# Kernel optimization log

Hardware: AMD Instinct MI355X
Metric: run time of the kernel (lower is better)

## Reference

```python
import jax, jax.numpy as jnp
import numpy as np

L, B, E = 512, 4, 256
SCALE = 0.05  # keep sigmoid in a non-saturated range


def setup_inputs() -> dict:
    key = jax.random.key(0)
    ks = jax.random.split(key, 6)
    return {
        "emb": jax.random.normal(ks[0], (L, B, E), dtype=jnp.float32),
        "w1": jax.random.normal(ks[1], (E, E), dtype=jnp.float32) * SCALE,
        "w2": jax.random.normal(ks[2], (E, E), dtype=jnp.float32) * SCALE,
        "w3": jax.random.normal(ks[3], (E, E), dtype=jnp.float32) * SCALE,
        "b3": jax.random.normal(ks[4], (E,), dtype=jnp.float32) * SCALE,
        "w0": jax.random.normal(ks[5], (E,), dtype=jnp.float32) * SCALE,
    }


def reference(emb, w1, w2, w3, b3, w0):
    # emb: (L, B, E). torch Linear computes x @ W.T (+ b).
    Lq = emb.shape[0]
    u = jnp.einsum('lbe,fe->lbf', emb, w1)                      # w1(x_i), per key i
    q = jnp.einsum('lbe,fe->lbf', emb, w2)                      # w2(x_t), per query t
    c = jnp.einsum('lbe,fe->lbf', jnp.cumsum(emb, axis=0), w3) + b3  # w3(cumsum up to t)
    # gate[t, i, b, e] = sigmoid(u[i] + q[t] + c[t]); additive score via w0
    gate = jax.nn.sigmoid(u[None, :, :, :] + (q + c)[:, None, :, :])  # (L, L, B, E)
    scores = jnp.einsum('tibe,e->tib', gate, w0)                # (L, L, B)
    causal = jnp.tril(jnp.ones((Lq, Lq), dtype=emb.dtype))      # i <= t
    scores = scores * causal[:, :, None]
    # m_a[t] = sum_{i<=t} a_i * x_i
    return jnp.einsum('tib,ibe->tbe', scores, emb)              # (L, B, E)
```

## Files before the change

### kernel.cpp

```cpp
#include <hip/hip_runtime.h>
#include <hip/hip_bf16.h>

#define L_  512
#define B_  4
#define E_  256
#define TT  8
#define TI  64
#define CH  16
#define ROWS_PER_CH (L_ / CH)

typedef unsigned short u16;

#define NLOG2E (-1.44269504f)

__device__ __forceinline__ float bflo(unsigned u) { return __uint_as_float(u << 16); }
__device__ __forceinline__ float bfhi(unsigned u) { return __uint_as_float(u & 0xffff0000u); }

__device__ __forceinline__ unsigned pack_bf2(float x, float y) {
  __hip_bfloat162 h = __float22bfloat162_rn(make_float2(x, y));
  return *reinterpret_cast<unsigned*>(&h);
}

__device__ __forceinline__ float sigs(float xs) {
  float e = __builtin_amdgcn_exp2f(xs);
  return __builtin_amdgcn_rcpf(1.0f + e);
}

__global__ __launch_bounds__(256) void gemm3_k(
    const float* __restrict__ A,
    const float* __restrict__ w1, const float* __restrict__ w2, const float* __restrict__ w3,
    float* __restrict__ o1, float* __restrict__ o2, float* __restrict__ o3) {
  __shared__ float As[64 * 32], Ws[64 * 32];
  const int tid = threadIdx.x, tx = tid & 15, ty = tid >> 4;
  const int r0 = blockIdx.x * 64, f0 = blockIdx.y * 64, z = blockIdx.z;
  const float* W = (z == 0) ? w1 : (z == 1) ? w2 : w3;
  float* O = (z == 0) ? o1 : (z == 1) ? o2 : o3;
  float acc[4][4] = {};
  for (int kb = 0; kb < 256; kb += 32) {
    for (int j = 0; j < 2; ++j) {
      int idx = j * 256 + tid;
      int r = idx >> 3, g = idx & 7;
      float4 av = *(const float4*)(A + (size_t)(r0 + r) * E_ + kb + g * 4);
      float4 wv = *(const float4*)(W + (size_t)(f0 + r) * E_ + kb + g * 4);
      int gs = g ^ ((r >> 2) & 7);
      *(float4*)(As + r * 32 + gs * 4) = av;
      *(float4*)(Ws + r * 32 + gs * 4) = wv;
    }
    __syncthreads();
#pragma unroll
    for (int g = 0; g < 8; ++g) {
      float4 a[4], w[4];
#pragma unroll
      for (int i = 0; i < 4; ++i) {
        int r = ty * 4 + i;
        a[i] = *(const float4*)(As + r * 32 + (g ^ ((r >> 2) & 7)) * 4);
        int f = tx * 4 + i;
        w[i] = *(const float4*)(Ws + f * 32 + (g ^ ((f >> 2) & 7)) * 4);
      }
#pragma unroll
      for (int i = 0; i < 4; ++i)
#pragma unroll
        for (int j = 0; j < 4; ++j)
          acc[i][j] += a[i].x * w[j].x + a[i].y * w[j].y + a[i].z * w[j].z + a[i].w * w[j].w;
    }
    __syncthreads();
  }
  const float scl = (z == 0) ? NLOG2E : 1.0f;
#pragma unroll
  for (int i = 0; i < 4; ++i) {
    float4 v = make_float4(acc[i][0] * scl, acc[i][1] * scl, acc[i][2] * scl, acc[i][3] * scl);
    *(float4*)(O + (size_t)(r0 + ty * 4 + i) * E_ + f0 + tx * 4) = v;
  }
}

__global__ __launch_bounds__(256) void scanA_k(
    const float* __restrict__ v3, float* __restrict__ tot) {
  const int e = threadIdx.x, c = blockIdx.x, b = blockIdx.y;
  float s = 0.f;
  for (int l = c * ROWS_PER_CH; l < (c + 1) * ROWS_PER_CH; ++l)
    s += v3[((size_t)l * B_ + b) * E_ + e];
  tot[((size_t)c * B_ + b) * E_ + e] = s;
}

__global__ __launch_bounds__(256) void scanB_k(
    const float* __restrict__ v3, float* __restrict__ q2qc,
    const float* __restrict__ b3, const float* __restrict__ tot) {
  const int e = threadIdx.x, c = blockIdx.x, b = blockIdx.y;
  float run = 0.f;
  for (int cc = 0; cc < c; ++cc)
    run += tot[((size_t)cc * B_ + b) * E_ + e];
  const float bb = b3[e];
  for (int l = c * ROWS_PER_CH; l < (c + 1) * ROWS_PER_CH; ++l) {
    size_t o = ((size_t)l * B_ + b) * E_ + e;
    run += v3[o];
    q2qc[o] = NLOG2E * (q2qc[o] + bb + run);
  }
}

__device__ __forceinline__ void stage_tile_bf16(const float* __restrict__ src_base,
                                                u16* tile, int tid) {
#pragma unroll
  for (int c = 0; c < 16; ++c) {
    int idx = c * 256 + tid;
    int r = idx >> 6, col4 = idx & 63;
    float4 v = *(const float4*)(src_base + (size_t)r * (B_ * E_) + col4 * 4);
    unsigned p0 = pack_bf2(v.x, v.y);
    unsigned p1 = pack_bf2(v.z, v.w);
    *(uint2*)(tile + r * 264 + col4 * 4) = make_uint2(p0, p1);
  }
}

__global__ __launch_bounds__(256) void attn_main_k(
    const float* __restrict__ emb, const float* __restrict__ U,
    const float* __restrict__ QC, const float* __restrict__ w0g,
    float* __restrict__ out) {
  const int tt = blockIdx.x, ic = blockIdx.y, b = blockIdx.z;
  const int t0 = tt * TT, i0 = ic * TI;
  if (i0 > t0 + TT - 1) return;

  __shared__ u16 tile[TI * 264];
  __shared__ float s_s[TT][TI];
  const int tid = threadIdx.x;
  const int wave = tid >> 6, lane = tid & 63;

  stage_tile_bf16(U + ((size_t)i0 * B_ + b) * E_, tile, tid);
  __syncthreads();

#pragma unroll
  for (int tl = 0; tl < 2; ++tl) {
    int t = t0 + wave * 2 + tl;
    float acc0 = 0.f, acc1 = 0.f, acc2 = 0.f, acc3 = 0.f;
    if (t >= i0) {
      int row = __builtin_amdgcn_readfirstlane(t * B_ + b);
      const float* qcrow = QC + (size_t)row * E_;
      const u16* urow = tile + lane * 264;
#pragma unroll 4
      for (int g = 0; g < 32; ++g) {
        uint4 raw = *(const uint4*)(urow + g * 8);
        float4 q0 = *(const float4*)(qcrow + g * 8);
        float4 q1 = *(const float4*)(qcrow + g * 8 + 4);
        float4 z0 = *(const float4*)(w0g + g * 8);
        float4 z1 = *(const float4*)(w0g + g * 8 + 4);
        acc0 += z0.x * sigs(bflo(raw.x) + q0.x);
        acc1 += z0.y * sigs(bfhi(raw.x) + q0.y);
        acc2 += z0.z * sigs(bflo(raw.y) + q0.z);
        acc3 += z0.w * sigs(bfhi(raw.y) + q0.w);
        acc0 += z1.x * sigs(bflo(raw.z) + q1.x);
        acc1 += z1.y * sigs(bfhi(raw.z) + q1.y);
        acc2 += z1.z * sigs(bflo(raw.w) + q1.z);
        acc3 += z1.w * sigs(bfhi(raw.w) + q1.w);
      }
    }
    float s = (acc0 + acc1) + (acc2 + acc3);
    if (i0 + lane > t) s = 0.f;
    s_s[wave * 2 + tl][lane] = s;
  }
  __syncthreads();

  stage_tile_bf16(emb + ((size_t)i0 * B_ + b) * E_, tile, tid);
  __syncthreads();

#pragma unroll
  for (int tl = 0; tl < 2; ++tl) {
    int t = t0 + wave * 2 + tl;
    if (t < i0) continue;
    float4 o = make_float4(0.f, 0.f, 0.f, 0.f);
    const int nI = min(TI, t - i0 + 1);
    const float* srow = &s_s[wave * 2 + tl][0];
    for (int i = 0; i < nI; ++i) {
      float s = srow[i];
      uint2 raw = *(const uint2*)(tile + i * 264 + lane * 4);
      o.x += s * bflo(raw.x);
      o.y += s * bfhi(raw.x);
      o.z += s * bflo(raw.y);
      o.w += s * bfhi(raw.y);
    }
    float* op = out + ((size_t)t * B_ + b) * E_ + lane * 4;
    atomicAdd(op + 0, o.x);
    atomicAdd(op + 1, o.y);
    atomicAdd(op + 2, o.z);
    atomicAdd(op + 3, o.w);
  }
}

extern "C" void kernel_launch(void* const* d_in, const int* in_sizes, int n_in,
                              void* d_out, int out_size, void* d_ws, size_t ws_size,
                              hipStream_t stream) {
  const float* emb = (const float*)d_in[0];
  const float* w1  = (const float*)d_in[1];
  const float* w2  = (const float*)d_in[2];
  const float* w3  = (const float*)d_in[3];
  const float* b3  = (const float*)d_in[4];
  const float* w0  = (const float*)d_in[5];
  float* out = (float*)d_out;

  float* U   = (float*)d_ws;
  float* Q2  = U + 524288;
  float* V3  = Q2 + 524288;
  float* TOT = V3 + 524288;

  hipMemsetAsync(out, 0, (size_t)524288 * sizeof(float), stream);
  gemm3_k<<<dim3(32, 4, 3), 256, 0, stream>>>(emb, w1, w2, w3, U, Q2, V3);
  scanA_k<<<dim3(CH, B_), 256, 0, stream>>>(V3, TOT);
  scanB_k<<<dim3(CH, B_), 256, 0, stream>>>(V3, Q2, b3, TOT);
  attn_main_k<<<dim3(L_ / TT, L_ / TI, B_), 256, 0, stream>>>(emb, U, Q2, w0, out);
}
```

Baseline: 171.4 us.

## Fuse the two-pass scan into one kernel and restructure the attention inner loops

```diff
diff --git a/kernel.cpp b/kernel.cpp
--- a/kernel.cpp
+++ b/kernel.cpp
@@ -6,11 +6,8 @@
 #define E_  256
 #define TT  8
 #define TI  64
-#define CH  16
-#define ROWS_PER_CH (L_ / CH)
 
 typedef unsigned short u16;
-
 #define NLOG2E (-1.44269504f)
 
 __device__ __forceinline__ float bflo(unsigned u) { return __uint_as_float(u << 16); }
@@ -73,40 +70,38 @@
   }
 }
 
-__global__ __launch_bounds__(256) void scanA_k(
-    const float* __restrict__ v3, float* __restrict__ tot) {
-  const int e = threadIdx.x, c = blockIdx.x, b = blockIdx.y;
-  float s = 0.f;
-  for (int l = c * ROWS_PER_CH; l < (c + 1) * ROWS_PER_CH; ++l)
-    s += v3[((size_t)l * B_ + b) * E_ + e];
-  tot[((size_t)c * B_ + b) * E_ + e] = s;
-}
-
-__global__ __launch_bounds__(256) void scanB_k(
-    const float* __restrict__ v3, float* __restrict__ q2qc,
-    const float* __restrict__ b3, const float* __restrict__ tot) {
-  const int e = threadIdx.x, c = blockIdx.x, b = blockIdx.y;
-  float run = 0.f;
-  for (int cc = 0; cc < c; ++cc)
-    run += tot[((size_t)cc * B_ + b) * E_ + e];
-  const float bb = b3[e];
-  for (int l = c * ROWS_PER_CH; l < (c + 1) * ROWS_PER_CH; ++l) {
-    size_t o = ((size_t)l * B_ + b) * E_ + e;
-    run += v3[o];
-    q2qc[o] = NLOG2E * (q2qc[o] + bb + run);
-  }
-}
-
-__device__ __forceinline__ void stage_tile_bf16(const float* __restrict__ src_base,
-                                                u16* tile, int tid) {
-#pragma unroll
-  for (int c = 0; c < 16; ++c) {
-    int idx = c * 256 + tid;
-    int r = idx >> 6, col4 = idx & 63;
-    float4 v = *(const float4*)(src_base + (size_t)r * (B_ * E_) + col4 * 4);
-    unsigned p0 = pack_bf2(v.x, v.y);
-    unsigned p1 = pack_bf2(v.z, v.w);
-    *(uint2*)(tile + r * 264 + col4 * 4) = make_uint2(p0, p1);
+__global__ __launch_bounds__(256) void scan_k(
+    const float* __restrict__ v3, float* __restrict__ q2qc, const float* __restrict__ b3g) {
+  const int bc = blockIdx.x;
+  const int cg = threadIdx.x & 3;
+  const int rk = threadIdx.x >> 2;
+  const int C = bc * 16 + cg * 4;
+  __shared__ float4 s_p[64][4];
+  float4 part = {0.f, 0.f, 0.f, 0.f};
+  for (int l = rk * 8; l < rk * 8 + 8; ++l) {
+    float4 v = *(const float4*)(v3 + (size_t)l * 1024 + C);
+    part.x += v.x; part.y += v.y; part.z += v.z; part.w += v.w;
+  }
+  s_p[rk][cg] = part;
+  __syncthreads();
+  float4 run = {0.f, 0.f, 0.f, 0.f};
+  for (int k = 0; k < rk; ++k) {
+    float4 p = s_p[k][cg];
+    run.x += p.x; run.y += p.y; run.z += p.z; run.w += p.w;
+  }
+  const int e = C & 255;
+  float4 bb = *(const float4*)(b3g + e);
+  for (int l = rk * 8; l < rk * 8 + 8; ++l) {
+    size_t o = (size_t)l * 1024 + C;
+    float4 v = *(const float4*)(v3 + o);
+    run.x += v.x; run.y += v.y; run.z += v.z; run.w += v.w;
+    float4 q = *(const float4*)(q2qc + o);
+    float4 r;
+    r.x = NLOG2E * (q.x + bb.x + run.x);
+    r.y = NLOG2E * (q.y + bb.y + run.y);
+    r.z = NLOG2E * (q.z + bb.z + run.z);
+    r.w = NLOG2E * (q.w + bb.w + run.w);
+    *(float4*)(q2qc + o) = r;
   }
 }
 
@@ -116,70 +111,82 @@
     float* __restrict__ out) {
   const int tt = blockIdx.x, ic = blockIdx.y, b = blockIdx.z;
   const int t0 = tt * TT, i0 = ic * TI;
-  if (i0 > t0 + TT - 1) return;
+  if (i0 > t0) return;
 
   __shared__ u16 tile[TI * 264];
   __shared__ float s_s[TT][TI];
-  const int tid = threadIdx.x;
-  const int wave = tid >> 6, lane = tid & 63;
-
-  stage_tile_bf16(U + ((size_t)i0 * B_ + b) * E_, tile, tid);
+  const int tid = threadIdx.x, wave = tid >> 6, lane = tid & 63;
+
+  {
+    const float* src = U + ((size_t)i0 * B_ + b) * E_ + lane * 4;
+#pragma unroll
+    for (int c = 0; c < 16; ++c) {
+      int r = c * 4 + wave;
+      float4 v = *(const float4*)(src + (size_t)r * (B_ * E_));
+      *(uint2*)(tile + r * 264 + lane * 4) =
+          make_uint2(pack_bf2(v.x, v.y), pack_bf2(v.z, v.w));
+    }
+  }
   __syncthreads();
 
-#pragma unroll
-  for (int tl = 0; tl < 2; ++tl) {
-    int t = t0 + wave * 2 + tl;
-    float acc0 = 0.f, acc1 = 0.f, acc2 = 0.f, acc3 = 0.f;
-    if (t >= i0) {
-      int row = __builtin_amdgcn_readfirstlane(t * B_ + b);
-      const float* qcrow = QC + (size_t)row * E_;
-      const u16* urow = tile + lane * 264;
+  const int tA = t0 + wave * 2, tB = tA + 1;
+  {
+    int rA = __builtin_amdgcn_readfirstlane(tA * B_ + b);
+    int rB = __builtin_amdgcn_readfirstlane(tB * B_ + b);
+    const float* qA = QC + (size_t)rA * E_;
+    const float* qB = QC + (size_t)rB * E_;
+    const u16* urow = tile + lane * 264;
+    float a0 = 0.f, a1 = 0.f, a2 = 0.f, a3 = 0.f;
+    float c0 = 0.f, c1 = 0.f, c2 = 0.f, c3 = 0.f;
 #pragma unroll 4
-      for (int g = 0; g < 32; ++g) {
-        uint4 raw = *(const uint4*)(urow + g * 8);
-        float4 q0 = *(const float4*)(qcrow + g * 8);
-        float4 q1 = *(const float4*)(qcrow + g * 8 + 4);
-        float4 z0 = *(const float4*)(w0g + g * 8);
-        float4 z1 = *(const float4*)(w0g + g * 8 + 4);
-        acc0 += z0.x * sigs(bflo(raw.x) + q0.x);
-        acc1 += z0.y * sigs(bfhi(raw.x) + q0.y);
-        acc2 += z0.z * sigs(bflo(raw.y) + q0.z);
-        acc3 += z0.w * sigs(bfhi(raw.y) + q0.w);
-        acc0 += z1.x * sigs(bflo(raw.z) + q1.x);
-        acc1 += z1.y * sigs(bfhi(raw.z) + q1.y);
-        acc2 += z1.z * sigs(bflo(raw.w) + q1.z);
-        acc3 += z1.w * sigs(bfhi(raw.w) + q1.w);
+    for (int g = 0; g < 32; ++g) {
+      uint4 raw = *(const uint4*)(urow + g * 8);
+      float4 z0 = *(const float4*)(w0g + g * 8);
+      float4 z1 = *(const float4*)(w0g + g * 8 + 4);
+      float4 qa0 = *(const float4*)(qA + g * 8);
+      float4 qa1 = *(const float4*)(qA + g * 8 + 4);
+      float4 qb0 = *(const float4*)(qB + g * 8);
+      float4 qb1 = *(const float4*)(qB + g * 8 + 4);
+      float u0 = bflo(raw.x), u1 = bfhi(raw.x), u2 = bflo(raw.y), u3 = bfhi(raw.y);
+      float u4 = bflo(raw.z), u5 = bfhi(raw.z), u6 = bflo(raw.w), u7 = bfhi(raw.w);
+      a0 += z0.x * sigs(u0 + qa0.x); a1 += z0.y * sigs(u1 + qa0.y);
+      a2 += z0.z * sigs(u2 + qa0.z); a3 += z0.w * sigs(u3 + qa0.w);
+      a0 += z1.x * sigs(u4 + qa1.x); a1 += z1.y * sigs(u5 + qa1.y);
+      a2 += z1.z * sigs(u6 + qa1.z); a3 += z1.w * sigs(u7 + qa1.w);
+      c0 += z0.x * sigs(u0 + qb0.x); c1 += z0.y * sigs(u1 + qb0.y);
+      c2 += z0.z * sigs(u2 + qb0.z); c3 += z0.w * sigs(u3 + qb0.w);
+      c0 += z1.x * sigs(u4 + qb1.x); c1 += z1.y * sigs(u5 + qb1.y);
+      c2 += z1.z * sigs(u6 + qb1.z); c3 += z1.w * sigs(u7 + qb1.w);
+    }
+    float sA = (a0 + a1) + (a2 + a3), sB = (c0 + c1) + (c2 + c3);
+    int i = i0 + lane;
+    s_s[wave * 2][lane]     = (i <= tA) ? sA : 0.f;
+    s_s[wave * 2 + 1][lane] = (i <= tB) ? sB : 0.f;
+  }
+  __syncthreads();
+
+  {
+    const float* embp = emb + ((size_t)i0 * B_ + b) * E_ + lane * 4;
+    const float* sAv = s_s[wave * 2];
+    const float* sBv = s_s[wave * 2 + 1];
+    int nI = min(TI, tB - i0 + 1);
+    nI = (nI + 3) & ~3;
+    float4 o0 = {0.f, 0.f, 0.f, 0.f}, o1 = {0.f, 0.f, 0.f, 0.f};
+    for (int i = 0; i < nI; i += 4) {
+#pragma unroll
+      for (int k = 0; k < 4; ++k) {
+        float4 r = *(const float4*)(embp + (size_t)(i + k) * (B_ * E_));
+        float s0 = sAv[i + k], s1 = sBv[i + k];
+        o0.x += s0 * r.x; o0.y += s0 * r.y; o0.z += s0 * r.z; o0.w += s0 * r.w;
+        o1.x += s1 * r.x; o1.y += s1 * r.y; o1.z += s1 * r.z; o1.w += s1 * r.w;
       }
     }
-    float s = (acc0 + acc1) + (acc2 + acc3);
-    if (i0 + lane > t) s = 0.f;
-    s_s[wave * 2 + tl][lane] = s;
-  }
-  __syncthreads();
-
-  stage_tile_bf16(emb + ((size_t)i0 * B_ + b) * E_, tile, tid);
-  __syncthreads();
-
-#pragma unroll
-  for (int tl = 0; tl < 2; ++tl) {
-    int t = t0 + wave * 2 + tl;
-    if (t < i0) continue;
-    float4 o = make_float4(0.f, 0.f, 0.f, 0.f);
-    const int nI = min(TI, t - i0 + 1);
-    const float* srow = &s_s[wave * 2 + tl][0];
-    for (int i = 0; i < nI; ++i) {
-      float s = srow[i];
-      uint2 raw = *(const uint2*)(tile + i * 264 + lane * 4);
-      o.x += s * bflo(raw.x);
-      o.y += s * bfhi(raw.x);
-      o.z += s * bflo(raw.y);
-      o.w += s * bfhi(raw.y);
-    }
-    float* op = out + ((size_t)t * B_ + b) * E_ + lane * 4;
-    atomicAdd(op + 0, o.x);
-    atomicAdd(op + 1, o.y);
-    atomicAdd(op + 2, o.z);
-    atomicAdd(op + 3, o.w);
+    float* opA = out + ((size_t)tA * B_ + b) * E_ + lane * 4;
+    float* opB = out + ((size_t)tB * B_ + b) * E_ + lane * 4;
+    atomicAdd(opA + 0, o0.x); atomicAdd(opA + 1, o0.y);
+    atomicAdd(opA + 2, o0.z); atomicAdd(opA + 3, o0.w);
+    atomicAdd(opB + 0, o1.x); atomicAdd(opB + 1, o1.y);
+    atomicAdd(opB + 2, o1.z); atomicAdd(opB + 3, o1.w);
   }
 }
 
@@ -194,14 +201,12 @@
   const float* w0  = (const float*)d_in[5];
   float* out = (float*)d_out;
 
-  float* U   = (float*)d_ws;
-  float* Q2  = U + 524288;
-  float* V3  = Q2 + 524288;
-  float* TOT = V3 + 524288;
+  float* U  = (float*)d_ws;
+  float* Q2 = U + 524288;
+  float* V3 = Q2 + 524288;
 
   hipMemsetAsync(out, 0, (size_t)524288 * sizeof(float), stream);
   gemm3_k<<<dim3(32, 4, 3), 256, 0, stream>>>(emb, w1, w2, w3, U, Q2, V3);
-  scanA_k<<<dim3(CH, B_), 256, 0, stream>>>(V3, TOT);
-  scanB_k<<<dim3(CH, B_), 256, 0, stream>>>(V3, Q2, b3, TOT);
+  scan_k<<<dim3(64), 256, 0, stream>>>(V3, Q2, b3);
   attn_main_k<<<dim3(L_ / TT, L_ / TI, B_), 256, 0, stream>>>(emb, U, Q2, w0, out);
 }
```

Result: faster. 152.6 us (-11.0%).
